# Kernel optimization log

Hardware: AMD Instinct MI355X
Metric: run time of the kernel (lower is better)

The kernel has to match this reference:

```python
import jax, jax.numpy as jnp
import numpy as np

B, T, H = 64, 256, 128

def setup_inputs() -> dict:
    key = jax.random.key(0)
    ks = jax.random.split(key, 10)
    s = 1.0 / np.sqrt(H)
    return {
        "x": jax.random.normal(ks[0], (B, T, 2), jnp.float32),
        "enc_output": jax.random.normal(ks[1], (B, T, H), jnp.float32),
        "h0": jax.random.normal(ks[2], (B, H), jnp.float32) * s,
        "c0": jax.random.normal(ks[3], (B, H), jnp.float32) * s,
        "W1": jax.random.normal(ks[4], (H, H), jnp.float32) * s,
        "W2": jax.random.normal(ks[5], (H, H), jnp.float32) * s,
        "V": jax.random.normal(ks[6], (H,), jnp.float32) * s,
        "Wk": jax.random.normal(ks[7], (2, 4 * H), jnp.float32) * (1.0 / np.sqrt(2.0)),
        "Wr": jax.random.normal(ks[8], (H, 4 * H), jnp.float32) * s,
        "b": jnp.zeros((4 * H,), jnp.float32),
    }


def reference(x, enc_output, h0, c0, W1, W2, V, Wk, Wr, b):
    Bb, Tt, _ = x.shape
    # Precompute W1 @ enc_output once (original recomputes it T times inside K.rnn)
    enc_proj = jnp.einsum('bth,hk->btk', enc_output, W1)  # [B,T,H]

    def lstm_cell(inp, h, c):
        # Keras LSTMCell, gate order i,f,c,o; sigmoid recurrent activation, tanh activation
        z = inp @ Wk + h @ Wr + b  # [B,4H]
        zi, zf, zg, zo = jnp.split(z, 4, axis=-1)
        i = jax.nn.sigmoid(zi)
        f = jax.nn.sigmoid(zf)
        g = jnp.tanh(zg)
        o = jax.nn.sigmoid(zo)
        c_new = f * c + i * g
        h_new = o * jnp.tanh(c_new)
        return h_new, c_new

    def step(carry, _):
        h, c, ptr = carry
        h, c = lstm_cell(ptr, h, c)
        # additive attention over all encoder steps, batched (replaces inner K.rnn)
        scores = jnp.einsum('btk,k->bt', jnp.tanh(enc_proj + (h @ W2)[:, None, :]), V)
        probs = jax.nn.softmax(scores, axis=1)  # [B,T]
        # get_pointer with rank=0: top-1 of descending argsort == argmax
        idx = jnp.argmax(probs, axis=1)  # [B]
        ptr = jnp.take_along_axis(x, idx[:, None, None], axis=1)[:, 0, :]  # [B,2]
        return (h, c, ptr), probs

    ptr0 = jnp.ones((Bb, 2), x.dtype)
    _, probs_seq = jax.lax.scan(step, (h0, c0, ptr0), None, length=Tt)  # [T,B,T]
    return jnp.transpose(probs_seq, (1, 0, 2))  # [B,T,T]
```

## Files before the change

kernel.cpp:

```cpp
#include <hip/hip_runtime.h>
#include <cstddef>

#define TT 256
#define HH 128
#define EST 132

__device__ __forceinline__ float rdlane(float v, int l) {
  return __int_as_float(__builtin_amdgcn_readlane(__float_as_int(v), l));
}
__device__ __forceinline__ float fast_sigmoid(float x) {
  const float L2E = 1.4426950408889634f;
  float y = __builtin_amdgcn_exp2f(-x * L2E);
  return __builtin_amdgcn_rcpf(1.0f + y);
}
__device__ __forceinline__ float fast_tanh(float x) {
  const float C2 = 2.8853900817779268f;
  float y = __builtin_amdgcn_exp2f(x * C2);
  return 1.0f - 2.0f * __builtin_amdgcn_rcpf(1.0f + y);
}

__global__ __launch_bounds__(512, 2)
void decoder_kernel(const float* __restrict__ x,
                    const float* __restrict__ enc_output,
                    const float* __restrict__ h0,
                    const float* __restrict__ c0,
                    const float* __restrict__ W1,
                    const float* __restrict__ W2,
                    const float* __restrict__ V,
                    const float* __restrict__ Wk,
                    const float* __restrict__ Wr,
                    const float* __restrict__ bias,
                    float* __restrict__ out)
{
  __shared__ float E[TT * EST];
  __shared__ float zpart[4 * 512];
  __shared__ float part[8][64];
  __shared__ float scp[8 * 257];
  __shared__ float hbuf[HH];
  __shared__ float xloc[TT * 2];
  __shared__ float amax_s[4];
  __shared__ int   amax_t[4];
  __shared__ float ssum[4];

  const int u    = threadIdx.x;
  const int b    = blockIdx.x;
  const int lane = u & 63;
  const int w    = u >> 6;
  const float C2  = 2.8853900817779268f;
  const float L2E = 1.4426950408889634f;

  {
    const float* encb = enc_output + (size_t)b * TT * HH;
    const int tsub = u >> 4;
    const int ks   = (u & 15) * 8;
    for (int p = 0; p < 8; ++p) {
      const int tt = p * 32 + tsub;
      float4 a0 = {0.f, 0.f, 0.f, 0.f};
      float4 a1 = {0.f, 0.f, 0.f, 0.f};
      const float4* er4 = (const float4*)(encb + tt * HH);
      for (int j4 = 0; j4 < 32; ++j4) {
        const float4 ev = er4[j4];
        const float* w1p = W1 + (j4 * 4) * HH + ks;
        float4 wa, wb;
        wa = *(const float4*)(w1p + 0 * HH); wb = *(const float4*)(w1p + 0 * HH + 4);
        a0.x += ev.x * wa.x; a0.y += ev.x * wa.y; a0.z += ev.x * wa.z; a0.w += ev.x * wa.w;
        a1.x += ev.x * wb.x; a1.y += ev.x * wb.y; a1.z += ev.x * wb.z; a1.w += ev.x * wb.w;
        wa = *(const float4*)(w1p + 1 * HH); wb = *(const float4*)(w1p + 1 * HH + 4);
        a0.x += ev.y * wa.x; a0.y += ev.y * wa.y; a0.z += ev.y * wa.z; a0.w += ev.y * wa.w;
        a1.x += ev.y * wb.x; a1.y += ev.y * wb.y; a1.z += ev.y * wb.z; a1.w += ev.y * wb.w;
        wa = *(const float4*)(w1p + 2 * HH); wb = *(const float4*)(w1p + 2 * HH + 4);
        a0.x += ev.z * wa.x; a0.y += ev.z * wa.y; a0.z += ev.z * wa.z; a0.w += ev.z * wa.w;
        a1.x += ev.z * wb.x; a1.y += ev.z * wb.y; a1.z += ev.z * wb.z; a1.w += ev.z * wb.w;
        wa = *(const float4*)(w1p + 3 * HH); wb = *(const float4*)(w1p + 3 * HH + 4);
        a0.x += ev.w * wa.x; a0.y += ev.w * wa.y; a0.z += ev.w * wa.z; a0.w += ev.w * wa.w;
        a1.x += ev.w * wb.x; a1.y += ev.w * wb.y; a1.z += ev.w * wb.z; a1.w += ev.w * wb.w;
      }
      *(float4*)(&E[tt * EST + ks])     = a0;
      *(float4*)(&E[tt * EST + ks + 4]) = a1;
    }
  }
  xloc[u] = x[b * (TT * 2) + u];
  if (u < HH) hbuf[u] = h0[b * HH + u];

  const int kq = u >> 7;
  const int cs = u & 127;
  float4 wr4[32];
  #pragma unroll
  for (int i = 0; i < 32; ++i)
    wr4[i] = *(const float4*)(Wr + (32 * kq + i) * 512 + 4 * cs);
  const int g = u & 3;
  const int m = u >> 2;
  const int col = g * HH + m;
  const float wk0 = Wk[col];
  const float wk1 = Wk[512 + col];
  const float bb  = bias[col];
  const int halfC = w & 1;
  const int tqC   = w >> 1;
  float w2col[32];
  #pragma unroll
  for (int jj = 0; jj < 32; ++jj)
    w2col[jj] = W2[(32 * tqC + jj) * HH + 64 * halfC + lane];
  const int kstar = 16 * w + (lane & 15);
  const int pD    = kstar >> 6;
  const int lD    = kstar & 63;
  const float v2r = -2.0f * V[kstar];
  float c = c0[b * HH + m];
  float ptr0 = 1.0f, ptr1 = 1.0f;
  float svr;
  {
    float v = V[lane] + V[64 + lane];
    #pragma unroll
    for (int o = 1; o < 64; o <<= 1) v += __shfl_xor(v, o, 64);
    svr = v;
  }

  __syncthreads();

  {
    float* Er = &E[(u >> 1) * EST + 64 * (u & 1)];
    #pragma unroll
    for (int i = 0; i < 16; ++i) {
      float4 ev = *(const float4*)(Er + 4 * i);
      ev.x = __builtin_amdgcn_exp2f(ev.x * C2);
      ev.y = __builtin_amdgcn_exp2f(ev.y * C2);
      ev.z = __builtin_amdgcn_exp2f(ev.z * C2);
      ev.w = __builtin_amdgcn_exp2f(ev.w * C2);
      *(float4*)(Er + 4 * i) = ev;
    }
  }
  float vL[16];
  #pragma unroll
  for (int i = 0; i < 16; ++i) vL[i] = rdlane(v2r, i);

  float hA = hbuf[32 * kq + (lane & 31)];
  float hC = hbuf[32 * tqC + (lane & 31)];
  {
    float4 zac = {0.f, 0.f, 0.f, 0.f};
    #pragma unroll
    for (int i = 0; i < 32; ++i) {
      float hi = rdlane(hA, i);
      zac.x += hi * wr4[i].x;
      zac.y += hi * wr4[i].y;
      zac.z += hi * wr4[i].z;
      zac.w += hi * wr4[i].w;
    }
    *(float4*)(&zpart[kq * 512 + 4 * cs]) = zac;
  }
  __syncthreads();

  float* outb = out + (size_t)b * TT * TT;

  #pragma unroll 1
  for (int step = 0; step < TT; ++step) {
    {
      float z = bb + ptr0 * wk0 + ptr1 * wk1;
      z += (zpart[0 * 512 + col] + zpart[1 * 512 + col]) +
           (zpart[2 * 512 + col] + zpart[3 * 512 + col]);
      float za = __shfl_xor(z, 1);
      float zb = __shfl_xor(z, 2);
      float zc = __shfl_xor(za, 2);
      float zi = (g == 0) ? z  : (g == 1) ? za : (g == 2) ? zb : zc;
      float zf = (g == 0) ? za : (g == 1) ? z  : (g == 2) ? zc : zb;
      float zg = (g == 0) ? zb : (g == 1) ? zc : (g == 2) ? z  : za;
      float zo = (g == 0) ? zc : (g == 1) ? zb : (g == 2) ? za : z;
      float ig = fast_sigmoid(zi);
      float fg = fast_sigmoid(zf);
      float gg = fast_tanh(zg);
      float og = fast_sigmoid(zo);
      c = fg * c + ig * gg;
      float hn = og * fast_tanh(c);
      if (g == 0) hbuf[m] = hn;
    }
    __syncthreads();
    hA = hbuf[32 * kq + (lane & 31)];
    hC = hbuf[32 * tqC + (lane & 31)];

    {
      float cp0 = 0.0f, cp1 = 0.0f;
      #pragma unroll
      for (int jj = 0; jj < 32; jj += 2) {
        cp0 += rdlane(hC, jj)     * w2col[jj];
        cp1 += rdlane(hC, jj + 1) * w2col[jj + 1];
      }
      part[w][lane] = cp0 + cp1;
    }
    __syncthreads();

    float Uk;
    {
      float usum = (part[pD][lD] + part[pD + 2][lD]) +
                   (part[pD + 4][lD] + part[pD + 6][lD]);
      Uk = __builtin_amdgcn_exp2f(usum * C2);
    }
    {
      float uL[16];
      #pragma unroll
      for (int i = 0; i < 16; ++i) uL[i] = rdlane(Uk, i);
      #pragma unroll
      for (int tt = 0; tt < 4; ++tt) {
        const float* Er = &E[(64 * tt + lane) * EST + 16 * w];
        float4 e0 = *(const float4*)(Er + 0);
        float4 e1 = *(const float4*)(Er + 4);
        float4 e2 = *(const float4*)(Er + 8);
        float4 e3 = *(const float4*)(Er + 12);
        float a0 = 0.0f, a1 = 0.0f;
        float t0, t1, n;
        t0 = fmaf(e0.x, uL[ 0], 1.0f); t1 = fmaf(e0.y, uL[ 1], 1.0f);
        n  = fmaf(vL[ 1], t0, vL[ 0] * t1);
        a0 = fmaf(n, __builtin_amdgcn_rcpf(t0 * t1), a0);
        t0 = fmaf(e0.z, uL[ 2], 1.0f); t1 = fmaf(e0.w, uL[ 3], 1.0f);
        n  = fmaf(vL[ 3], t0, vL[ 2] * t1);
        a1 = fmaf(n, __builtin_amdgcn_rcpf(t0 * t1), a1);
        t0 = fmaf(e1.x, uL[ 4], 1.0f); t1 = fmaf(e1.y, uL[ 5], 1.0f);
        n  = fmaf(vL[ 5], t0, vL[ 4] * t1);
        a0 = fmaf(n, __builtin_amdgcn_rcpf(t0 * t1), a0);
        t0 = fmaf(e1.z, uL[ 6], 1.0f); t1 = fmaf(e1.w, uL[ 7], 1.0f);
        n  = fmaf(vL[ 7], t0, vL[ 6] * t1);
        a1 = fmaf(n, __builtin_amdgcn_rcpf(t0 * t1), a1);
        t0 = fmaf(e2.x, uL[ 8], 1.0f); t1 = fmaf(e2.y, uL[ 9], 1.0f);
        n  = fmaf(vL[ 9], t0, vL[ 8] * t1);
        a0 = fmaf(n, __builtin_amdgcn_rcpf(t0 * t1), a0);
        t0 = fmaf(e2.z, uL[10], 1.0f); t1 = fmaf(e2.w, uL[11], 1.0f);
        n  = fmaf(vL[11], t0, vL[10] * t1);
        a1 = fmaf(n, __builtin_amdgcn_rcpf(t0 * t1), a1);
        t0 = fmaf(e3.x, uL[12], 1.0f); t1 = fmaf(e3.y, uL[13], 1.0f);
        n  = fmaf(vL[13], t0, vL[12] * t1);
        a0 = fmaf(n, __builtin_amdgcn_rcpf(t0 * t1), a0);
        t0 = fmaf(e3.z, uL[14], 1.0f); t1 = fmaf(e3.w, uL[15], 1.0f);
        n  = fmaf(vL[15], t0, vL[14] * t1);
        a1 = fmaf(n, __builtin_amdgcn_rcpf(t0 * t1), a1);
        scp[w * 257 + 64 * tt + lane] = a0 + a1;
      }
    }
    {
      float4 zac = {0.f, 0.f, 0.f, 0.f};
      #pragma unroll
      for (int i = 0; i < 32; ++i) {
        float hi = rdlane(hA, i);
        zac.x += hi * wr4[i].x;
        zac.y += hi * wr4[i].y;
        zac.z += hi * wr4[i].z;
        zac.w += hi * wr4[i].w;
      }
      *(float4*)(&zpart[kq * 512 + 4 * cs]) = zac;
    }
    __syncthreads();

    float p = 0.0f;
    if (u < 256) {
      float s0 = 0.0f, s1 = 0.0f;
      #pragma unroll
      for (int q = 0; q < 8; q += 2) {
        s0 += scp[q * 257 + u];
        s1 += scp[(q + 1) * 257 + u];
      }
      float score = svr + s0 + s1;
      p = __builtin_amdgcn_exp2f((score - 12.0f) * L2E);
      float mx = score;
      float wsv = p;
      #pragma unroll
      for (int o = 1; o < 64; o <<= 1) {
        mx = fmaxf(mx, __shfl_xor(mx, o));
        wsv += __shfl_xor(wsv, o);
      }
      unsigned long long bal = __ballot(score == mx);
      int bt = 64 * w + (__ffsll(bal) - 1);
      if (lane == 0) { amax_s[w] = mx; amax_t[w] = bt; ssum[w] = wsv; }
    }
    __syncthreads();

    float fbs = amax_s[0]; int fbt = amax_t[0];
    #pragma unroll
    for (int q = 1; q < 4; ++q) {
      float s2v = amax_s[q]; int t2v = amax_t[q];
      if (s2v > fbs || (s2v == fbs && t2v < fbt)) { fbs = s2v; fbt = t2v; }
    }
    float sumtot = (ssum[0] + ssum[1]) + (ssum[2] + ssum[3]);
    ptr0 = xloc[2 * fbt + 0];
    ptr1 = xloc[2 * fbt + 1];
    if (u < 256) outb[(size_t)step * TT + u] = p * __builtin_amdgcn_rcpf(sumtot);
  }
}

extern "C" void kernel_launch(void* const* d_in, const int* in_sizes, int n_in,
                              void* d_out, int out_size, void* d_ws, size_t ws_size,
                              hipStream_t stream) {
  (void)in_sizes; (void)n_in; (void)d_ws; (void)ws_size; (void)out_size;
  const float* x    = (const float*)d_in[0];
  const float* enc  = (const float*)d_in[1];
  const float* h0   = (const float*)d_in[2];
  const float* c0   = (const float*)d_in[3];
  const float* W1   = (const float*)d_in[4];
  const float* W2   = (const float*)d_in[5];
  const float* V    = (const float*)d_in[6];
  const float* Wk   = (const float*)d_in[7];
  const float* Wr   = (const float*)d_in[8];
  const float* bias = (const float*)d_in[9];
  float* out = (float*)d_out;

  decoder_kernel<<<64, 512, 0, stream>>>(x, enc, h0, c0, W1, W2, V, Wk, Wr, bias, out);
}
```

Baseline: 870.0 us.

## Merge softmax/argmax into next step's LSTM phase and drop a barrier

Each of waves 0-3 now reduces all 256 scores itself with shuffles, so every wave knows the full argmax and softmax sum without going through shared memory. That reduction, plus the output store, is deferred to the start of the next step, ahead of the LSTM update. The LSTM update now runs on 128 threads that each handle four gates, which removes the gate shuffles. The Wr matvec moves ahead of the attention phase, cutting per-step barriers from four to three at the cost of redundant reduction work across four waves and an epilogue for the last step.

```diff
diff --git a/kernel.cpp b/kernel.cpp
--- a/kernel.cpp
+++ b/kernel.cpp
@@ -38,9 +38,6 @@
   __shared__ float scp[8 * 257];
   __shared__ float hbuf[HH];
   __shared__ float xloc[TT * 2];
-  __shared__ float amax_s[4];
-  __shared__ int   amax_t[4];
-  __shared__ float ssum[4];
 
   const int u    = threadIdx.x;
   const int b    = blockIdx.x;
@@ -80,7 +77,6 @@
     }
   }
   xloc[u] = x[b * (TT * 2) + u];
-  if (u < HH) hbuf[u] = h0[b * HH + u];
 
   const int kq = u >> 7;
   const int cs = u & 127;
@@ -88,12 +84,15 @@
   #pragma unroll
   for (int i = 0; i < 32; ++i)
     wr4[i] = *(const float4*)(Wr + (32 * kq + i) * 512 + 4 * cs);
-  const int g = u & 3;
-  const int m = u >> 2;
-  const int col = g * HH + m;
-  const float wk0 = Wk[col];
-  const float wk1 = Wk[512 + col];
-  const float bb  = bias[col];
+  const int m = u & 127;
+  float wkA[4], wkB[4], bbg[4];
+  #pragma unroll
+  for (int gg = 0; gg < 4; ++gg) {
+    wkA[gg] = Wk[gg * HH + m];
+    wkB[gg] = Wk[512 + gg * HH + m];
+    bbg[gg] = bias[gg * HH + m];
+  }
+  float c = c0[b * HH + m];
   const int halfC = w & 1;
   const int tqC   = w >> 1;
   float w2col[32];
@@ -104,7 +103,6 @@
   const int pD    = kstar >> 6;
   const int lD    = kstar & 63;
   const float v2r = -2.0f * V[kstar];
-  float c = c0[b * HH + m];
   float ptr0 = 1.0f, ptr1 = 1.0f;
   float svr;
   {
@@ -131,14 +129,12 @@
   float vL[16];
   #pragma unroll
   for (int i = 0; i < 16; ++i) vL[i] = rdlane(v2r, i);
-
-  float hA = hbuf[32 * kq + (lane & 31)];
-  float hC = hbuf[32 * tqC + (lane & 31)];
   {
+    float hA0 = h0[(size_t)b * HH + 32 * kq + (lane & 31)];
     float4 zac = {0.f, 0.f, 0.f, 0.f};
     #pragma unroll
     for (int i = 0; i < 32; ++i) {
-      float hi = rdlane(hA, i);
+      float hi = rdlane(hA0, i);
       zac.x += hi * wr4[i].x;
       zac.y += hi * wr4[i].y;
       zac.z += hi * wr4[i].z;
@@ -152,29 +148,61 @@
 
   #pragma unroll 1
   for (int step = 0; step < TT; ++step) {
-    {
-      float z = bb + ptr0 * wk0 + ptr1 * wk1;
-      z += (zpart[0 * 512 + col] + zpart[1 * 512 + col]) +
-           (zpart[2 * 512 + col] + zpart[3 * 512 + col]);
-      float za = __shfl_xor(z, 1);
-      float zb = __shfl_xor(z, 2);
-      float zc = __shfl_xor(za, 2);
-      float zi = (g == 0) ? z  : (g == 1) ? za : (g == 2) ? zb : zc;
-      float zf = (g == 0) ? za : (g == 1) ? z  : (g == 2) ? zc : zb;
-      float zg = (g == 0) ? zb : (g == 1) ? zc : (g == 2) ? z  : za;
-      float zo = (g == 0) ? zc : (g == 1) ? zb : (g == 2) ? za : z;
-      float ig = fast_sigmoid(zi);
-      float fg = fast_sigmoid(zf);
-      float gg = fast_tanh(zg);
-      float og = fast_sigmoid(zo);
+    if (step > 0 && w < 4) {
+      float s0 = 0.f, s1 = 0.f, s2 = 0.f, s3 = 0.f;
+      #pragma unroll
+      for (int q = 0; q < 8; ++q) {
+        s0 += scp[q * 257 + 0 * 64 + lane];
+        s1 += scp[q * 257 + 1 * 64 + lane];
+        s2 += scp[q * 257 + 2 * 64 + lane];
+        s3 += scp[q * 257 + 3 * 64 + lane];
+      }
+      s0 += svr; s1 += svr; s2 += svr; s3 += svr;
+      float p0 = __builtin_amdgcn_exp2f((s0 - 12.0f) * L2E);
+      float p1 = __builtin_amdgcn_exp2f((s1 - 12.0f) * L2E);
+      float p2 = __builtin_amdgcn_exp2f((s2 - 12.0f) * L2E);
+      float p3 = __builtin_amdgcn_exp2f((s3 - 12.0f) * L2E);
+      float m4 = fmaxf(fmaxf(s0, s1), fmaxf(s2, s3));
+      int ttl = (s0 == m4) ? 0 : (s1 == m4) ? 1 : (s2 == m4) ? 2 : 3;
+      float ws4 = (p0 + p1) + (p2 + p3);
+      float mx = m4;
+      #pragma unroll
+      for (int o = 1; o < 64; o <<= 1) {
+        mx  = fmaxf(mx, __shfl_xor(mx, o));
+        ws4 += __shfl_xor(ws4, o);
+      }
+      unsigned long long bal = __ballot(m4 == mx);
+      int ls  = __ffsll((unsigned long long)bal) - 1;
+      int tts = __builtin_amdgcn_readlane(ttl, ls);
+      int fbt = 64 * tts + ls;
+      ptr0 = xloc[2 * fbt + 0];
+      ptr1 = xloc[2 * fbt + 1];
+      float pw = (w == 0) ? p0 : (w == 1) ? p1 : (w == 2) ? p2 : p3;
+      outb[(size_t)(step - 1) * TT + 64 * w + lane] = pw * __builtin_amdgcn_rcpf(ws4);
+    }
+    if (u < HH) {
+      float z0 = bbg[0] + ptr0 * wkA[0] + ptr1 * wkB[0];
+      float z1 = bbg[1] + ptr0 * wkA[1] + ptr1 * wkB[1];
+      float z2 = bbg[2] + ptr0 * wkA[2] + ptr1 * wkB[2];
+      float z3 = bbg[3] + ptr0 * wkA[3] + ptr1 * wkB[3];
+      #pragma unroll
+      for (int q = 0; q < 4; ++q) {
+        z0 += zpart[q * 512 + 0 * HH + m];
+        z1 += zpart[q * 512 + 1 * HH + m];
+        z2 += zpart[q * 512 + 2 * HH + m];
+        z3 += zpart[q * 512 + 3 * HH + m];
+      }
+      float ig = fast_sigmoid(z0);
+      float fg = fast_sigmoid(z1);
+      float gg = fast_tanh(z2);
+      float og = fast_sigmoid(z3);
       c = fg * c + ig * gg;
-      float hn = og * fast_tanh(c);
-      if (g == 0) hbuf[m] = hn;
+      hbuf[m] = og * fast_tanh(c);
     }
     __syncthreads();
-    hA = hbuf[32 * kq + (lane & 31)];
-    hC = hbuf[32 * tqC + (lane & 31)];
-
+
+    float hC = hbuf[32 * tqC + (lane & 31)];
+    float hA = hbuf[32 * kq  + (lane & 31)];
     {
       float cp0 = 0.0f, cp1 = 0.0f;
       #pragma unroll
@@ -183,6 +211,18 @@
         cp1 += rdlane(hC, jj + 1) * w2col[jj + 1];
       }
       part[w][lane] = cp0 + cp1;
+    }
+    {
+      float4 zac = {0.f, 0.f, 0.f, 0.f};
+      #pragma unroll
+      for (int i = 0; i < 32; ++i) {
+        float hi = rdlane(hA, i);
+        zac.x += hi * wr4[i].x;
+        zac.y += hi * wr4[i].y;
+        zac.z += hi * wr4[i].z;
+        zac.w += hi * wr4[i].w;
+      }
+      *(float4*)(&zpart[kq * 512 + 4 * cs]) = zac;
     }
     __syncthreads();
 
@@ -232,53 +272,28 @@
         scp[w * 257 + 64 * tt + lane] = a0 + a1;
       }
     }
-    {
-      float4 zac = {0.f, 0.f, 0.f, 0.f};
-      #pragma unroll
-      for (int i = 0; i < 32; ++i) {
-        float hi = rdlane(hA, i);
-        zac.x += hi * wr4[i].x;
-        zac.y += hi * wr4[i].y;
-        zac.z += hi * wr4[i].z;
-        zac.w += hi * wr4[i].w;
-      }
-      *(float4*)(&zpart[kq * 512 + 4 * cs]) = zac;
-    }
     __syncthreads();
-
-    float p = 0.0f;
-    if (u < 256) {
-      float s0 = 0.0f, s1 = 0.0f;
-      #pragma unroll
-      for (int q = 0; q < 8; q += 2) {
-        s0 += scp[q * 257 + u];
-        s1 += scp[(q + 1) * 257 + u];
-      }
-      float score = svr + s0 + s1;
-      p = __builtin_amdgcn_exp2f((score - 12.0f) * L2E);
-      float mx = score;
-      float wsv = p;
-      #pragma unroll
-      for (int o = 1; o < 64; o <<= 1) {
-        mx = fmaxf(mx, __shfl_xor(mx, o));
-        wsv += __shfl_xor(wsv, o);
-      }
-      unsigned long long bal = __ballot(score == mx);
-      int bt = 64 * w + (__ffsll(bal) - 1);
-      if (lane == 0) { amax_s[w] = mx; amax_t[w] = bt; ssum[w] = wsv; }
-    }
-    __syncthreads();
-
-    float fbs = amax_s[0]; int fbt = amax_t[0];
-    #pragma unroll
-    for (int q = 1; q < 4; ++q) {
-      float s2v = amax_s[q]; int t2v = amax_t[q];
-      if (s2v > fbs || (s2v == fbs && t2v < fbt)) { fbs = s2v; fbt = t2v; }
-    }
-    float sumtot = (ssum[0] + ssum[1]) + (ssum[2] + ssum[3]);
-    ptr0 = xloc[2 * fbt + 0];
-    ptr1 = xloc[2 * fbt + 1];
-    if (u < 256) outb[(size_t)step * TT + u] = p * __builtin_amdgcn_rcpf(sumtot);
+  }
+
+  if (w < 4) {
+    float s0 = 0.f, s1 = 0.f, s2 = 0.f, s3 = 0.f;
+    #pragma unroll
+    for (int q = 0; q < 8; ++q) {
+      s0 += scp[q * 257 + 0 * 64 + lane];
+      s1 += scp[q * 257 + 1 * 64 + lane];
+      s2 += scp[q * 257 + 2 * 64 + lane];
+      s3 += scp[q * 257 + 3 * 64 + lane];
+    }
+    s0 += svr; s1 += svr; s2 += svr; s3 += svr;
+    float p0 = __builtin_amdgcn_exp2f((s0 - 12.0f) * L2E);
+    float p1 = __builtin_amdgcn_exp2f((s1 - 12.0f) * L2E);
+    float p2 = __builtin_amdgcn_exp2f((s2 - 12.0f) * L2E);
+    float p3 = __builtin_amdgcn_exp2f((s3 - 12.0f) * L2E);
+    float ws4 = (p0 + p1) + (p2 + p3);
+    #pragma unroll
+    for (int o = 1; o < 64; o <<= 1) ws4 += __shfl_xor(ws4, o);
+    float pw = (w == 0) ? p0 : (w == 1) ? p1 : (w == 2) ? p2 : p3;
+    outb[(size_t)255 * TT + 64 * w + lane] = pw * __builtin_amdgcn_rcpf(ws4);
   }
 }
 
```

After: 841.5 us. 1.03x faster.
